# Kernel optimization log

Measured on AMD Instinct MI355X. Metric: run time of the kernel, lower is better.

The kernel has to match this reference:

```python
import jax, jax.numpy as jnp
import numpy as np

B, NPER, H = 32, 512, 32
N, E = B * NPER, 65536
IN_CH, EDGE_CH, L1, L2, NL = 100, 16, 64, 64, 4


def setup_inputs() -> dict:
    key = jax.random.key(0)
    ks = jax.random.split(key, 14)
    f = lambda k, s: jax.random.normal(k, s, dtype=jnp.float32) * 0.1
    return {
        "x_nodes": jax.random.randint(ks[0], (N,), 0, IN_CH),
        "edge_index": jax.random.randint(ks[1], (2, E), 0, N),
        "edge_attr": jax.random.randint(ks[2], (E,), 0, EDGE_CH),
        "metal_idx": jax.random.randint(ks[3], (B,), 0, NPER),
        "loop_edge": jax.random.randint(ks[4], (B, L1, 2), 0, NPER),
        "loop_pair": jax.random.randint(ks[5], (B, L2, 2), 0, NPER),
        "node_emb": f(ks[6], (IN_CH, H)),
        "edge_emb": f(ks[7], (NL, EDGE_CH, 8)),
        "lin_w": f(ks[8], (NL, 8, H * H)),
        "lin_b": f(ks[9], (NL, H * H)),
        "root_w": f(ks[10], (NL, H, H)),
        "conv_b": f(ks[11], (NL, H)),
        "f_w": f(ks[12], (H, 1)),
        "f_b": f(ks[13], (1,)),
    }


def reference(x_nodes, edge_index, edge_attr, metal_idx, loop_edge, loop_pair,
              node_emb, edge_emb, lin_w, lin_b, root_w, conv_b, f_w, f_b):
    src, dst = edge_index[0], edge_index[1]
    # mean-aggregation denominator (clamped to 1 for isolated nodes, as PyG)
    deg = jax.ops.segment_sum(jnp.ones((E,), jnp.float32), dst, num_segments=N)
    denom = jnp.maximum(deg, 1.0)[:, None]

    x = node_emb[x_nodes]  # [N,H]
    for l in range(NL):
        # edge nn: Embedding -> ReLU -> Linear(8, H*H)
        e8 = jax.nn.relu(edge_emb[l][edge_attr])              # [E,8]
        W = (e8 @ lin_w[l] + lin_b[l]).reshape(E, H, H)       # [E,H,H]
        msg = jnp.einsum('ei,eio->eo', x[src], W)             # [E,H]
        agg = jax.ops.segment_sum(msg, dst, num_segments=N) / denom
        x_new = agg + x @ root_w[l] + conv_b[l]               # root weight + bias
        x = jax.nn.relu(x_new) if l < NL - 1 else x_new

    metal_g = metal_idx + jnp.arange(B) * NPER                # global metal node ids
    xm = x[metal_g]                                           # [B,H]
    fhM = (xm @ f_w + f_b)[:, 0]                              # [B]

    xg = x.reshape(B, NPER, H)
    bidx = jnp.arange(B)[:, None]

    def pair_prod(pairs):
        xs = xg[bidx, pairs[:, :, 0]]                         # [B,L,H]
        xt = xg[bidx, pairs[:, :, 1]]                         # [B,L,H]
        # sum(xm*xs) + sum(xm*xt) + sum(xs*(-xt))
        return jnp.sum(xm[:, None, :] * (xs + xt) - xs * xt, axis=-1)

    res_edge = pair_prod(loop_edge) - fhM[:, None]            # [B,L1]
    res_pair = -pair_prod(loop_pair)                          # [B,L2]
    return jnp.concatenate([res_edge, res_pair], axis=1)      # [B, L1+L2]
```

## Files before the change

kernel.cpp:

```cpp
#include <hip/hip_runtime.h>

#define NN 16384
#define NE 65536
#define H  32
#define BB 32
#define NPERB 512

__global__ void k_prep(const int* __restrict__ x_nodes, const int* __restrict__ edge_index,
                       const int* __restrict__ edge_attr,
                       const float* __restrict__ node_emb, const float* __restrict__ edge_emb,
                       const float* __restrict__ lin_w, const float* __restrict__ lin_b,
                       float* __restrict__ x0, float* __restrict__ Wt,
                       unsigned int* __restrict__ packed, float* __restrict__ degf,
                       float* __restrict__ zbuf) {
    int t = blockIdx.x * 256 + threadIdx.x;
    if (t < 524288) {
        int n = t >> 5, h = t & 31;
        x0[t] = node_emb[x_nodes[n] * H + h];
    } else if (t < 589824) {
        int w = t - 524288;
        int l = w >> 14, rest = w & 16383;
        int ty = rest >> 10, io = rest & 1023;
        float acc = lin_b[l * 1024 + io];
#pragma unroll
        for (int j = 0; j < 8; ++j) {
            float e = edge_emb[(l * 16 + ty) * 8 + j];
            e = e > 0.f ? e : 0.f;
            acc = fmaf(e, lin_w[(l * 8 + j) * 1024 + io], acc);
        }
        Wt[w] = acc;
    } else if (t < 655360) {
        int e = t - 589824;
        unsigned int s  = (unsigned int)edge_index[e];
        unsigned int d  = (unsigned int)edge_index[NE + e];
        unsigned int ty = (unsigned int)edge_attr[e];
        packed[e] = s | (d << 14) | (ty << 28);
        atomicAdd(&degf[d], 1.0f);
    } else {
        zbuf[t - 655360] = 0.f;
    }
}

__global__ void k_phase(const float* __restrict__ xin, float* __restrict__ xout,
                        float* __restrict__ zbuf,
                        const unsigned int* __restrict__ packed, const float* __restrict__ degf,
                        const float* __restrict__ Wt_l, const float* __restrict__ root_l,
                        const float* __restrict__ b_l, int relu_in) {
    int t = blockIdx.x * 256 + threadIdx.x;
    int base = threadIdx.x & 32;
    if (t < 2097152) {
        int e = t >> 5, o = t & 31;
        unsigned int p = packed[e];
        int s  = p & 16383;
        int d  = (p >> 14) & 16383;
        int ty = p >> 28;
        float xv = xin[s * H + o];
        if (relu_in) xv = xv > 0.f ? xv : 0.f;
        float invd = __builtin_amdgcn_rcpf(fmaxf(degf[d], 1.0f));
        const float* __restrict__ W = Wt_l + ty * 1024 + o;
        float acc = 0.f;
#pragma unroll
        for (int i = 0; i < 32; ++i)
            acc = fmaf(__shfl(xv, base + i), W[i * 32], acc);
        atomicAdd(&xout[d * H + o], acc * invd);
    } else if (t < 2621440) {
        int t2 = t - 2097152;
        int o = t2 & 31;
        float xv = xin[t2];
        if (relu_in) xv = xv > 0.f ? xv : 0.f;
        float acc = b_l[o];
#pragma unroll
        for (int i = 0; i < 32; ++i)
            acc = fmaf(__shfl(xv, base + i), root_l[i * 32 + o], acc);
        atomicAdd(&xout[t2], acc);
    } else if (zbuf) {
        zbuf[t - 2621440] = 0.f;
    }
}

__global__ void k_final(const float* __restrict__ x, const int* __restrict__ metal_idx,
                        const int* __restrict__ loop_edge, const int* __restrict__ loop_pair,
                        const float* __restrict__ f_w, const float* __restrict__ f_b,
                        float* __restrict__ out) {
    int tid = blockIdx.x * blockDim.x + threadIdx.x;
    if (tid >= BB * 128) return;
    int b = tid >> 7, j = tid & 127;
    int mg = metal_idx[b] + b * NPERB;
    const float* __restrict__ xm = x + mg * H;
    int p0, p1;
    if (j < 64) {
        p0 = loop_edge[(b * 64 + j) * 2];
        p1 = loop_edge[(b * 64 + j) * 2 + 1];
    } else {
        int j2 = j - 64;
        p0 = loop_pair[(b * 64 + j2) * 2];
        p1 = loop_pair[(b * 64 + j2) * 2 + 1];
    }
    const float* __restrict__ xs = x + (b * NPERB + p0) * H;
    const float* __restrict__ xt = x + (b * NPERB + p1) * H;
    float fh = f_b[0];
    float pp = 0.f;
#pragma unroll
    for (int h = 0; h < H; ++h) {
        float m = xm[h];
        fh = fmaf(m, f_w[h], fh);
        pp += m * (xs[h] + xt[h]) - xs[h] * xt[h];
    }
    out[tid] = (j < 64) ? (pp - fh) : (-pp);
}

extern "C" void kernel_launch(void* const* d_in, const int* in_sizes, int n_in,
                              void* d_out, int out_size, void* d_ws, size_t ws_size,
                              hipStream_t stream) {
    const int*   x_nodes    = (const int*)d_in[0];
    const int*   edge_index = (const int*)d_in[1];
    const int*   edge_attr  = (const int*)d_in[2];
    const int*   metal_idx  = (const int*)d_in[3];
    const int*   loop_edge  = (const int*)d_in[4];
    const int*   loop_pair  = (const int*)d_in[5];
    const float* node_emb   = (const float*)d_in[6];
    const float* edge_emb   = (const float*)d_in[7];
    const float* lin_w      = (const float*)d_in[8];
    const float* lin_b      = (const float*)d_in[9];
    const float* root_w     = (const float*)d_in[10];
    const float* conv_b     = (const float*)d_in[11];
    const float* f_w        = (const float*)d_in[12];
    const float* f_b        = (const float*)d_in[13];
    float* out = (float*)d_out;

    float* ws   = (float*)d_ws;
    float* buf0 = ws;
    float* buf1 = buf0 + NN * H;
    float* buf2 = buf1 + NN * H;
    float* degf = buf2 + NN * H;
    unsigned int* packed = (unsigned int*)(degf + NN);
    float* Wt   = (float*)(packed + NE);

    hipMemsetAsync(degf, 0, NN * sizeof(float), stream);

    k_prep<<<4608, 256, 0, stream>>>(x_nodes, edge_index, edge_attr, node_emb, edge_emb,
                                     lin_w, lin_b, buf0, Wt, packed, degf, buf1);

    k_phase<<<12288, 256, 0, stream>>>(buf0, buf1, buf2, packed, degf,
                                       Wt + 0 * 16384, root_w + 0 * 1024, conv_b + 0 * H, 0);
    k_phase<<<12288, 256, 0, stream>>>(buf1, buf2, buf0, packed, degf,
                                       Wt + 1 * 16384, root_w + 1 * 1024, conv_b + 1 * H, 1);
    k_phase<<<12288, 256, 0, stream>>>(buf2, buf0, buf1, packed, degf,
                                       Wt + 2 * 16384, root_w + 2 * 1024, conv_b + 2 * H, 1);
    k_phase<<<10240, 256, 0, stream>>>(buf0, buf1, (float*)0, packed, degf,
                                       Wt + 3 * 16384, root_w + 3 * 1024, conv_b + 3 * H, 1);

    k_final<<<16, 256, 0, stream>>>(buf1, metal_idx, loop_edge, loop_pair, f_w, f_b, out);
}
```

Measured before the change: 90.66 us.

## Bucket edges by type and compute 4 outputs per thread with float4 matvec

Edges are counting-sorted by edge type via three prep kernels (histogram, scan, scatter) so neighbouring threads share the same per-type weight matrix. Each thread now computes four output channels from a float4-loaded source row, replacing the 32-lane shuffle matvec, which cuts thread count by 4x. Extra launches and atomics in the prep add overhead, and the scattered edge order changes atomic add ordering and raises register use.

```diff
diff --git a/kernel.cpp b/kernel.cpp
--- a/kernel.cpp
+++ b/kernel.cpp
@@ -6,75 +6,129 @@
 #define BB 32
 #define NPERB 512
 
-__global__ void k_prep(const int* __restrict__ x_nodes, const int* __restrict__ edge_index,
-                       const int* __restrict__ edge_attr,
-                       const float* __restrict__ node_emb, const float* __restrict__ edge_emb,
-                       const float* __restrict__ lin_w, const float* __restrict__ lin_b,
-                       float* __restrict__ x0, float* __restrict__ Wt,
-                       unsigned int* __restrict__ packed, float* __restrict__ degf,
-                       float* __restrict__ zbuf) {
-    int t = blockIdx.x * 256 + threadIdx.x;
-    if (t < 524288) {
-        int n = t >> 5, h = t & 31;
-        x0[t] = node_emb[x_nodes[n] * H + h];
-    } else if (t < 589824) {
-        int w = t - 524288;
+__device__ __forceinline__ void matvec8(const float* __restrict__ xrow,
+                                        const float4* __restrict__ W4, int j,
+                                        int relu_in, float4& acc) {
+    const float4* __restrict__ xr4 = (const float4*)xrow;
+    float4 a0 = xr4[0], a1 = xr4[1], a2 = xr4[2], a3 = xr4[3],
+           a4 = xr4[4], a5 = xr4[5], a6 = xr4[6], a7 = xr4[7];
+    float xr[32];
+#define XC(k, v) xr[4*k+0]=v.x; xr[4*k+1]=v.y; xr[4*k+2]=v.z; xr[4*k+3]=v.w;
+    XC(0,a0) XC(1,a1) XC(2,a2) XC(3,a3) XC(4,a4) XC(5,a5) XC(6,a6) XC(7,a7)
+#undef XC
+    if (relu_in) {
+#pragma unroll
+        for (int k = 0; k < 32; ++k) xr[k] = fmaxf(xr[k], 0.f);
+    }
+#pragma unroll
+    for (int i = 0; i < 32; ++i) {
+        float4 w = W4[i * 8 + j];
+        acc.x = fmaf(xr[i], w.x, acc.x);
+        acc.y = fmaf(xr[i], w.y, acc.y);
+        acc.z = fmaf(xr[i], w.z, acc.z);
+        acc.w = fmaf(xr[i], w.w, acc.w);
+    }
+}
+
+__global__ __launch_bounds__(256) void k_prep1(
+    const int* __restrict__ x_nodes, const int* __restrict__ edge_index,
+    const int* __restrict__ edge_attr, const float* __restrict__ node_emb,
+    const float* __restrict__ edge_emb, const float* __restrict__ lin_w,
+    const float* __restrict__ lin_b, float* __restrict__ x0, float* __restrict__ Wt,
+    float* __restrict__ degf, int* __restrict__ tcount, float* __restrict__ zb1) {
+    __shared__ int lh[16];
+    int b = blockIdx.x, thr = threadIdx.x;
+    if (b < 512) {
+        int t = b * 256 + thr;
+        int n = t >> 3, r = t & 7;
+        int xn = x_nodes[n];
+        ((float4*)x0)[t] = ((const float4*)node_emb)[xn * 8 + r];
+    } else if (b < 768) {
+        int w = (b - 512) * 256 + thr;
         int l = w >> 14, rest = w & 16383;
         int ty = rest >> 10, io = rest & 1023;
         float acc = lin_b[l * 1024 + io];
 #pragma unroll
-        for (int j = 0; j < 8; ++j) {
-            float e = edge_emb[(l * 16 + ty) * 8 + j];
-            e = e > 0.f ? e : 0.f;
-            acc = fmaf(e, lin_w[(l * 8 + j) * 1024 + io], acc);
+        for (int jj = 0; jj < 8; ++jj) {
+            float e2 = fmaxf(edge_emb[(l * 16 + ty) * 8 + jj], 0.f);
+            acc = fmaf(e2, lin_w[(l * 8 + jj) * 1024 + io], acc);
         }
         Wt[w] = acc;
+    } else if (b < 1024) {
+        if (thr < 16) lh[thr] = 0;
+        __syncthreads();
+        int e = (b - 768) * 256 + thr;
+        int d = edge_index[NE + e];
+        int ty = edge_attr[e];
+        atomicAdd(&degf[d], 1.0f);
+        atomicAdd(&lh[ty], 1);
+        __syncthreads();
+        if (thr < 16) atomicAdd(&tcount[thr], lh[thr]);
+    } else {
+        int z = (b - 1024) * 256 + thr;
+        ((float4*)zb1)[z] = make_float4(0.f, 0.f, 0.f, 0.f);
+    }
+}
+
+__global__ void k_prep2(const int* __restrict__ tcount, int* __restrict__ gcursor) {
+    int t = threadIdx.x;
+    int c = (t < 16) ? tcount[t] : 0;
+    int base = 0;
+    for (int u = 0; u < 15; ++u) {
+        int cu = __shfl(c, u);
+        if (u < t) base += cu;
+    }
+    if (t < 16) gcursor[t] = base;
+}
+
+__global__ __launch_bounds__(256) void k_prep3(
+    const int* __restrict__ edge_index, const int* __restrict__ edge_attr,
+    int* __restrict__ gcursor, unsigned int* __restrict__ blist) {
+    __shared__ int lh[16], lb[16];
+    int thr = threadIdx.x;
+    if (thr < 16) lh[thr] = 0;
+    __syncthreads();
+    int e = blockIdx.x * 256 + thr;
+    unsigned int s = (unsigned int)edge_index[e];
+    unsigned int d = (unsigned int)edge_index[NE + e];
+    int ty = edge_attr[e];
+    int rank = atomicAdd(&lh[ty], 1);
+    __syncthreads();
+    if (thr < 16) lb[thr] = atomicAdd(&gcursor[thr], lh[thr]);
+    __syncthreads();
+    blist[lb[ty] + rank] = s | (d << 14) | ((unsigned int)ty << 28);
+}
+
+__global__ __launch_bounds__(256) void k_phase(
+    const float* __restrict__ xin, float* __restrict__ xout, float* __restrict__ zb,
+    const unsigned int* __restrict__ blist, const float* __restrict__ degf,
+    const float* __restrict__ Wl, const float* __restrict__ Rl,
+    const float* __restrict__ Bl, int relu_in) {
+    int t = blockIdx.x * 256 + threadIdx.x;
+    if (t < 524288) {
+        int e = t >> 3, j = t & 7;
+        unsigned int p = blist[e];
+        int s = p & 16383, d = (p >> 14) & 16383, ty = (int)(p >> 28);
+        float4 acc = make_float4(0.f, 0.f, 0.f, 0.f);
+        matvec8(xin + s * H, (const float4*)(Wl + ty * 1024), j, relu_in, acc);
+        float invd = __builtin_amdgcn_rcpf(fmaxf(degf[d], 1.0f));
+        float* o = xout + d * H + j * 4;
+        atomicAdd(o + 0, acc.x * invd);
+        atomicAdd(o + 1, acc.y * invd);
+        atomicAdd(o + 2, acc.z * invd);
+        atomicAdd(o + 3, acc.w * invd);
     } else if (t < 655360) {
-        int e = t - 589824;
-        unsigned int s  = (unsigned int)edge_index[e];
-        unsigned int d  = (unsigned int)edge_index[NE + e];
-        unsigned int ty = (unsigned int)edge_attr[e];
-        packed[e] = s | (d << 14) | (ty << 28);
-        atomicAdd(&degf[d], 1.0f);
-    } else {
-        zbuf[t - 655360] = 0.f;
-    }
-}
-
-__global__ void k_phase(const float* __restrict__ xin, float* __restrict__ xout,
-                        float* __restrict__ zbuf,
-                        const unsigned int* __restrict__ packed, const float* __restrict__ degf,
-                        const float* __restrict__ Wt_l, const float* __restrict__ root_l,
-                        const float* __restrict__ b_l, int relu_in) {
-    int t = blockIdx.x * 256 + threadIdx.x;
-    int base = threadIdx.x & 32;
-    if (t < 2097152) {
-        int e = t >> 5, o = t & 31;
-        unsigned int p = packed[e];
-        int s  = p & 16383;
-        int d  = (p >> 14) & 16383;
-        int ty = p >> 28;
-        float xv = xin[s * H + o];
-        if (relu_in) xv = xv > 0.f ? xv : 0.f;
-        float invd = __builtin_amdgcn_rcpf(fmaxf(degf[d], 1.0f));
-        const float* __restrict__ W = Wt_l + ty * 1024 + o;
-        float acc = 0.f;
-#pragma unroll
-        for (int i = 0; i < 32; ++i)
-            acc = fmaf(__shfl(xv, base + i), W[i * 32], acc);
-        atomicAdd(&xout[d * H + o], acc * invd);
-    } else if (t < 2621440) {
-        int t2 = t - 2097152;
-        int o = t2 & 31;
-        float xv = xin[t2];
-        if (relu_in) xv = xv > 0.f ? xv : 0.f;
-        float acc = b_l[o];
-#pragma unroll
-        for (int i = 0; i < 32; ++i)
-            acc = fmaf(__shfl(xv, base + i), root_l[i * 32 + o], acc);
-        atomicAdd(&xout[t2], acc);
-    } else if (zbuf) {
-        zbuf[t - 2621440] = 0.f;
+        int t2 = t - 524288;
+        int n = t2 >> 3, j = t2 & 7;
+        float4 acc = ((const float4*)Bl)[j];
+        matvec8(xin + n * H, (const float4*)Rl, j, relu_in, acc);
+        float* o = xout + n * H + j * 4;
+        atomicAdd(o + 0, acc.x);
+        atomicAdd(o + 1, acc.y);
+        atomicAdd(o + 2, acc.z);
+        atomicAdd(o + 3, acc.w);
+    } else if (zb) {
+        ((float4*)zb)[t - 655360] = make_float4(0.f, 0.f, 0.f, 0.f);
     }
 }
 
@@ -133,22 +187,26 @@
     float* buf1 = buf0 + NN * H;
     float* buf2 = buf1 + NN * H;
     float* degf = buf2 + NN * H;
-    unsigned int* packed = (unsigned int*)(degf + NN);
-    float* Wt   = (float*)(packed + NE);
-
-    hipMemsetAsync(degf, 0, NN * sizeof(float), stream);
-
-    k_prep<<<4608, 256, 0, stream>>>(x_nodes, edge_index, edge_attr, node_emb, edge_emb,
-                                     lin_w, lin_b, buf0, Wt, packed, degf, buf1);
-
-    k_phase<<<12288, 256, 0, stream>>>(buf0, buf1, buf2, packed, degf,
-                                       Wt + 0 * 16384, root_w + 0 * 1024, conv_b + 0 * H, 0);
-    k_phase<<<12288, 256, 0, stream>>>(buf1, buf2, buf0, packed, degf,
-                                       Wt + 1 * 16384, root_w + 1 * 1024, conv_b + 1 * H, 1);
-    k_phase<<<12288, 256, 0, stream>>>(buf2, buf0, buf1, packed, degf,
-                                       Wt + 2 * 16384, root_w + 2 * 1024, conv_b + 2 * H, 1);
-    k_phase<<<10240, 256, 0, stream>>>(buf0, buf1, (float*)0, packed, degf,
-                                       Wt + 3 * 16384, root_w + 3 * 1024, conv_b + 3 * H, 1);
+    int*   tcount  = (int*)(degf + NN);
+    int*   gcursor = tcount + 16;
+    unsigned int* blist = (unsigned int*)(gcursor + 16);
+    float* Wt   = (float*)(blist + NE);
+
+    hipMemsetAsync(degf, 0, (NN + 32) * sizeof(float), stream);
+
+    k_prep1<<<1536, 256, 0, stream>>>(x_nodes, edge_index, edge_attr, node_emb,
+                                      edge_emb, lin_w, lin_b, buf0, Wt, degf, tcount, buf1);
+    k_prep2<<<1, 64, 0, stream>>>(tcount, gcursor);
+    k_prep3<<<256, 256, 0, stream>>>(edge_index, edge_attr, gcursor, blist);
+
+    k_phase<<<3072, 256, 0, stream>>>(buf0, buf1, buf2, blist, degf,
+                                      Wt + 0 * 16384, root_w + 0 * 1024, conv_b + 0 * H, 0);
+    k_phase<<<3072, 256, 0, stream>>>(buf1, buf2, buf0, blist, degf,
+                                      Wt + 1 * 16384, root_w + 1 * 1024, conv_b + 1 * H, 1);
+    k_phase<<<3072, 256, 0, stream>>>(buf2, buf0, buf1, blist, degf,
+                                      Wt + 2 * 16384, root_w + 2 * 1024, conv_b + 2 * H, 1);
+    k_phase<<<2560, 256, 0, stream>>>(buf0, buf1, (float*)0, blist, degf,
+                                      Wt + 3 * 16384, root_w + 3 * 1024, conv_b + 3 * H, 1);
 
     k_final<<<16, 256, 0, stream>>>(buf1, metal_idx, loop_edge, loop_pair, f_w, f_b, out);
 }
```

After: 185.8 us. +104.9%, slower.
